# Kernel tuning notes

Measured on AMD Instinct MI355X. Metric: run time of the kernel, lower is better.

## Reference

```python
import jax, jax.numpy as jnp
import numpy as np
from jax import lax

EPS = 1e-5
K = 16  # MixedOp.self.k


def conv(x, w, stride=1, pad=0, dil=1, groups=1):
    return lax.conv_general_dilated(
        x, w, (stride, stride), [(pad, pad), (pad, pad)],
        rhs_dilation=(dil, dil), feature_group_count=groups,
        dimension_numbers=('NCHW', 'OIHW', 'NCHW'))


def bn(x):
    # BatchNorm2d(affine=False) in training mode: normalize with batch stats
    m = jnp.mean(x, axis=(0, 2, 3), keepdims=True)
    v = jnp.var(x, axis=(0, 2, 3), keepdims=True)
    return (x - m) * lax.rsqrt(v + EPS)


def maxpool3(x):
    return lax.reduce_window(x, -jnp.inf, lax.max, (1, 1, 3, 3), (1, 1, 1, 1),
                             [(0, 0), (0, 0), (1, 1), (1, 1)])


def avgpool3(x):
    # AvgPool2d(3, stride=1, padding=1, count_include_pad=False)
    s = lax.reduce_window(x, 0., lax.add, (1, 1, 3, 3), (1, 1, 1, 1),
                          [(0, 0), (0, 0), (1, 1), (1, 1)])
    c = lax.reduce_window(jnp.ones_like(x), 0., lax.add, (1, 1, 3, 3),
                          (1, 1, 1, 1), [(0, 0), (0, 0), (1, 1), (1, 1)])
    return s / c


def sep_conv(x, dw1, pw1, dw2, pw2):
    C = x.shape[1]
    p = dw1.shape[-1] // 2
    h = jax.nn.relu(x)
    h = conv(h, dw1, pad=p, groups=C)
    h = bn(conv(h, pw1))
    h = jax.nn.relu(h)
    h = conv(h, dw2, pad=p, groups=C)
    return bn(conv(h, pw2))


def dil_conv(x, dw, pw):
    C = x.shape[1]
    p = (dw.shape[-1] // 2) * 2  # dilation=2 padding (3x3->2, 5x5->4)
    h = jax.nn.relu(x)
    h = conv(h, dw, pad=p, dil=2, groups=C)
    return bn(conv(h, pw))


def setup_inputs() -> dict:
    key = jax.random.key(0)
    C, B, H, W = 256, 32, 64, 64
    c_op = C // K  # 16 channels fed to each candidate op
    ks = jax.random.split(key, 17)
    g = lambda k, shp, fan: jax.random.normal(k, shp, jnp.float32) / np.sqrt(fan)
    return {
        'x': jax.random.normal(ks[0], (B, C, H, W), jnp.float32),
        # ChannelAttention se: 1x1 convs, reduction=2
        'ca_w1': g(ks[1], (C // 2, C, 1, 1), C),
        'ca_w2': g(ks[2], (C, C // 2, 1, 1), C // 2),
        # sep_conv_3x3 (two dw+pw stages)
        's3_dw1': g(ks[3], (c_op, 1, 3, 3), 9),
        's3_pw1': g(ks[4], (c_op, c_op, 1, 1), c_op),
        's3_dw2': g(ks[5], (c_op, 1, 3, 3), 9),
        's3_pw2': g(ks[6], (c_op, c_op, 1, 1), c_op),
        # sep_conv_5x5
        's5_dw1': g(ks[7], (c_op, 1, 5, 5), 25),
        's5_pw1': g(ks[8], (c_op, c_op, 1, 1), c_op),
        's5_dw2': g(ks[9], (c_op, 1, 5, 5), 25),
        's5_pw2': g(ks[10], (c_op, c_op, 1, 1), c_op),
        # dil_conv_3x3 / dil_conv_5x5
        'd3_dw': g(ks[11], (c_op, 1, 3, 3), 9),
        'd3_pw': g(ks[12], (c_op, c_op, 1, 1), c_op),
        'd5_dw': g(ks[13], (c_op, 1, 5, 5), 25),
        'd5_pw': g(ks[14], (c_op, c_op, 1, 1), c_op),
        # AttentionModule fc: channel = 8*c_op = 128, ratio = 8
        'at_w1': g(ks[15], (c_op, 8 * c_op), 8 * c_op),  # Linear(128->16)
        'at_w2': g(ks[16], (8 * c_op, c_op), c_op),      # Linear(16->128)
    }


def reference(x, ca_w1, ca_w2, s3_dw1, s3_pw1, s3_dw2, s3_pw2,
              s5_dw1, s5_pw1, s5_dw2, s5_pw2, d3_dw, d3_pw, d5_dw, d5_pw,
              at_w1, at_w2):
    B, C, H, W = x.shape
    c_sel = C // K  # number of selected channels (16)

    # ---- ChannelAttention ----
    mx = jnp.max(x, axis=(2, 3), keepdims=True)   # [B,C,1,1]
    av = jnp.mean(x, axis=(2, 3), keepdims=True)
    se = lambda z: conv(jax.nn.relu(conv(z, ca_w1)), ca_w2)
    num_list = jax.nn.sigmoid(se(mx) + se(av))    # [B,C,1,1]

    aux = x                                       # auxiliary_op = Identity (stride=1)
    xg = x * num_list

    # ---- top-k channel routing ----
    slist = jnp.sum(num_list, axis=0).reshape(C)  # sum over batch
    _, idx = lax.top_k(slist, c_sel)              # sorted, largest first
    xt = xg[:, idx]                               # gather [B,c_sel,H,W]

    # ---- 8 candidate branches (DARTS PRIMITIVES, stride=1) ----
    branches = [
        jnp.zeros_like(xt),                       # none
        bn(maxpool3(xt)),                         # max_pool_3x3 + BN
        bn(avgpool3(xt)),                         # avg_pool_3x3 + BN
        xt,                                       # skip_connect (Identity)
        sep_conv(xt, s3_dw1, s3_pw1, s3_dw2, s3_pw2),
        sep_conv(xt, s5_dw1, s5_pw1, s5_dw2, s5_pw2),
        dil_conv(xt, d3_dw, d3_pw),
        dil_conv(xt, d5_dw, d5_pw),
    ]
    temp = jnp.concatenate(branches, axis=1)      # [B, 8*c_sel, H, W]

    # ---- AttentionModule ----
    y = jnp.mean(temp, axis=(2, 3))               # [B, 8*c_sel]
    y = jax.nn.sigmoid(jax.nn.relu(y @ at_w1.T) @ at_w2.T)
    att = temp * y[:, :, None, None]
    op_attention = jnp.sum(y.reshape(B, 8, c_sel), axis=(0, 2))  # [8]

    # sum the 8 branch chunks
    out = jnp.sum(att.reshape(B, 8, c_sel, H, W), axis=1)

    # scatter back into gated x, then residual add
    xg = xg.at[:, idx].set(out)
    return xg + aux, op_attention
```

## Files before the change

### kernel.cpp

```cpp
#include <hip/hip_runtime.h>
#include <math.h>

static constexpr int B = 32, C = 256, HW = 4096, CS = 16;
static constexpr int BHW = B * HW;
static constexpr size_t IMG = (size_t)B * CS * HW;

static constexpr size_t OFF_S     = 0;
static constexpr size_t OFF_SQ    = 4096;
static constexpr size_t OFF_U     = 8192;
static constexpr size_t ACC_FLOATS= 8256;
static constexpr size_t OFF_MX    = 8256;
static constexpr size_t OFF_AV    = OFF_MX + 8192;
static constexpr size_t OFF_NUM   = OFF_AV + 8192;
static constexpr size_t OFF_Y     = OFF_NUM + 8192;
static constexpr size_t OFF_ACO   = OFF_Y + 4096;
static constexpr size_t OFF_BIAS  = OFF_ACO + 4096;
static constexpr size_t OFF_INT   = OFF_BIAS + 512;
static constexpr size_t OFF_R     = 42112;

__device__ inline float wave_sum(float v) {
  v += __shfl_down(v, 32); v += __shfl_down(v, 16); v += __shfl_down(v, 8);
  v += __shfl_down(v, 4);  v += __shfl_down(v, 2);  v += __shfl_down(v, 1);
  return v;
}
__device__ inline float wave_max(float v) {
  v = fmaxf(v, __shfl_down(v, 32)); v = fmaxf(v, __shfl_down(v, 16));
  v = fmaxf(v, __shfl_down(v, 8));  v = fmaxf(v, __shfl_down(v, 4));
  v = fmaxf(v, __shfl_down(v, 2));  v = fmaxf(v, __shfl_down(v, 1));
  return v;
}

__global__ __launch_bounds__(256) void k_stats(const float4* __restrict__ x,
                                               float* __restrict__ mx, float* __restrict__ av) {
  int bc = blockIdx.x;
  const float4* p = x + (size_t)bc * 1024;
  float mmax = -INFINITY, msum = 0.f;
  for (int i = threadIdx.x; i < 1024; i += 256) {
    float4 v = p[i];
    mmax = fmaxf(mmax, fmaxf(fmaxf(v.x, v.y), fmaxf(v.z, v.w)));
    msum += v.x + v.y + v.z + v.w;
  }
  __shared__ float rs[4], rm[4];
  float s = wave_sum(msum), m = wave_max(mmax);
  int w = threadIdx.x >> 6;
  if ((threadIdx.x & 63) == 0) { rs[w] = s; rm[w] = m; }
  __syncthreads();
  if (threadIdx.x == 0) {
    mx[bc] = fmaxf(fmaxf(rm[0], rm[1]), fmaxf(rm[2], rm[3]));
    av[bc] = (rs[0] + rs[1] + rs[2] + rs[3]) * (1.f / 4096.f);
  }
}

__global__ __launch_bounds__(128) void k_se(const float* __restrict__ mx, const float* __restrict__ av,
                                            const float* __restrict__ w1, const float* __restrict__ w2,
                                            float* __restrict__ num) {
  int b = blockIdx.x, t = threadIdx.x;
  __shared__ float zs[2][256], h[2][128];
  for (int i = t; i < 256; i += 128) { zs[0][i] = mx[b * 256 + i]; zs[1][i] = av[b * 256 + i]; }
  __syncthreads();
  {
    const float* wr = w1 + (size_t)t * 256;
    float am = 0.f, aa = 0.f;
    for (int i = 0; i < 256; i++) { float w = wr[i]; am = fmaf(w, zs[0][i], am); aa = fmaf(w, zs[1][i], aa); }
    h[0][t] = fmaxf(am, 0.f); h[1][t] = fmaxf(aa, 0.f);
  }
  __syncthreads();
  for (int c = t; c < 256; c += 128) {
    const float* wr = w2 + (size_t)c * 128;
    float sm = 0.f, sa = 0.f;
    for (int j = 0; j < 128; j++) { float w = wr[j]; sm = fmaf(w, h[0][j], sm); sa = fmaf(w, h[1][j], sa); }
    float s = sm + sa;
    num[b * 256 + c] = 1.f / (1.f + expf(-s));
  }
}

__global__ __launch_bounds__(256) void k_select(const float* __restrict__ num,
                                                int* __restrict__ idx, int* __restrict__ selmap,
                                                float* __restrict__ accbase) {
  __shared__ float s[256];
  int t = threadIdx.x;
  for (int i = t; i < (int)ACC_FLOATS; i += 256) accbase[i] = 0.f;
  float acc = 0.f;
  for (int b = 0; b < B; b++) acc += num[b * 256 + t];
  s[t] = acc; selmap[t] = -1;
  __syncthreads();
  float v = s[t];
  int rank = 0;
  for (int c = 0; c < 256; c++) {
    float o = s[c];
    rank += (o > v) || (o == v && c < t);
  }
  if (rank < 16) { idx[rank] = t; selmap[t] = rank; }
}

template<int KK, int DIL, int BN>
__device__ __forceinline__ void dw_full(const float* __restrict__ src, float sc,
                                        const float* __restrict__ w, float* __restrict__ dst,
                                        float* lt, float mu, float rs) {
  constexpr int P = (KK / 2) * DIL, TW = 64 + 2 * P;
  float wr[KK * KK];
#pragma unroll
  for (int i = 0; i < KK * KK; i++) wr[i] = w[i];
  for (int i = threadIdx.x; i < TW * TW; i += 256) {
    int ty = i / TW, tx = i - ty * TW;
    int y = ty - P, xx = tx - P;
    float v = 0.f;
    if ((unsigned)y < 64u && (unsigned)xx < 64u) {
      v = src[y * 64 + xx] * sc;
      if (BN) v = (v - mu) * rs;
      v = fmaxf(v, 0.f);
    }
    lt[i] = v;
  }
  __syncthreads();
  for (int i = threadIdx.x; i < HW; i += 256) {
    int y = i >> 6, xx = i & 63;
    const float* t0 = lt + y * TW + xx;
    float acc = 0.f;
#pragma unroll
    for (int a = 0; a < KK; a++)
#pragma unroll
      for (int q = 0; q < KK; q++)
        acc = fmaf(wr[a * KK + q], t0[a * DIL * TW + q * DIL], acc);
    dst[i] = acc;
  }
}

__device__ __forceinline__ void pools_full(const float* __restrict__ src, float sc,
                                           float* __restrict__ dmax, float* __restrict__ davg,
                                           float* __restrict__ S, float* __restrict__ SQ,
                                           int bk, float* lt, float* red) {
  for (int i = threadIdx.x; i < HW; i += 256) lt[i] = src[i] * sc;
  __syncthreads();
  float s1 = 0.f, q1 = 0.f, s2 = 0.f, q2 = 0.f, s3 = 0.f;
  for (int i = threadIdx.x; i < HW; i += 256) {
    int y = i >> 6, xx = i & 63;
    int y0 = max(y - 1, 0), y1 = min(y + 1, 63), x0 = max(xx - 1, 0), x1 = min(xx + 1, 63);
    float mx = -INFINITY, sm = 0.f;
    for (int yy = y0; yy <= y1; yy++)
      for (int cx = x0; cx <= x1; cx++) { float v = lt[yy * 64 + cx]; mx = fmaxf(mx, v); sm += v; }
    float av = sm / (float)((y1 - y0 + 1) * (x1 - x0 + 1));
    dmax[i] = mx; davg[i] = av;
    s1 += mx; q1 += mx * mx; s2 += av; q2 += av * av; s3 += lt[i];
  }
  s1 = wave_sum(s1); q1 = wave_sum(q1); s2 = wave_sum(s2); q2 = wave_sum(q2); s3 = wave_sum(s3);
  int w = threadIdx.x >> 6;
  if ((threadIdx.x & 63) == 0) { red[w] = s1; red[4 + w] = q1; red[8 + w] = s2; red[12 + w] = q2; red[16 + w] = s3; }
  __syncthreads();
  if (threadIdx.x == 0) {
    S[512 + bk]  = red[0] + red[1] + red[2] + red[3];
    SQ[512 + bk] = red[4] + red[5] + red[6] + red[7];
    S[1024 + bk] = red[8] + red[9] + red[10] + red[11];
    SQ[1024 + bk]= red[12] + red[13] + red[14] + red[15];
    S[1536 + bk] = red[16] + red[17] + red[18] + red[19];
  }
}

__global__ __launch_bounds__(256) void k_branchA(
    const float* __restrict__ x, const float* __restrict__ num, const int* __restrict__ idx,
    const float* __restrict__ d3dw, const float* __restrict__ d5dw,
    const float* __restrict__ s3dw1, const float* __restrict__ s5dw1,
    float* __restrict__ R, float* __restrict__ scr,
    float* __restrict__ S, float* __restrict__ SQ) {
  __shared__ float lt[72 * 72];
  __shared__ float red[20];
  int blk = blockIdx.x;
  int op = blk / 512, bk = blk - op * 512;
  int b = bk >> 4, k = bk & 15;
  int c = idx[k];
  float sc = num[b * 256 + c];
  const float* src = x + ((size_t)b * 256 + c) * HW;
  size_t o = (size_t)bk * HW;
  switch (op) {
    case 0: pools_full(src, sc, R + o, R + IMG + o, S, SQ, bk, lt, red); break;
    case 1: dw_full<3, 2, 0>(src, sc, d3dw + k * 9,  scr + 0 * IMG + o, lt, 0.f, 0.f); break;
    case 2: dw_full<5, 2, 0>(src, sc, d5dw + k * 25, scr + 1 * IMG + o, lt, 0.f, 0.f); break;
    case 3: dw_full<3, 1, 0>(src, sc, s3dw1 + k * 9,  scr + 2 * IMG + o, lt, 0.f, 0.f); break;
    case 4: dw_full<5, 1, 0>(src, sc, s5dw1 + k * 25, scr + 3 * IMG + o, lt, 0.f, 0.f); break;
  }
}

__device__ __forceinline__ void pw_tile(const float* __restrict__ in, const float* __restrict__ w16,
                                        float* __restrict__ out, float* __restrict__ sacc,
                                        float* __restrict__ qacc, int perB, int b, int tile,
                                        float* wsh, float* redS, float* redQ) {
  int t = threadIdx.x;
  wsh[t] = w16[t];
  size_t base = (size_t)b * 16 * HW + tile * 256;
  float sv[16];
#pragma unroll
  for (int i = 0; i < 16; i++) sv[i] = in[base + (size_t)i * HW + t];
  __syncthreads();
  int wv = t >> 6, lane = t & 63;
#pragma unroll
  for (int cc = 0; cc < 16; cc++) {
    float acc = 0.f;
#pragma unroll
    for (int i = 0; i < 16; i++) acc = fmaf(wsh[cc * 16 + i], sv[i], acc);
    out[base + (size_t)cc * HW + t] = acc;
    float s = wave_sum(acc), q = wave_sum(acc * acc);
    if (lane == 0) { redS[cc * 4 + wv] = s; redQ[cc * 4 + wv] = q; }
  }
  __syncthreads();
  if (t < 16) {
    float s = redS[t * 4] + redS[t * 4 + 1] + redS[t * 4 + 2] + redS[t * 4 + 3];
    float q = redQ[t * 4] + redQ[t * 4 + 1] + redQ[t * 4 + 2] + redQ[t * 4 + 3];
    int sl = perB ? b * 16 + t : t;
    atomicAdd(&sacc[sl], s); atomicAdd(&qacc[sl], q);
  }
}

__global__ __launch_bounds__(256) void k_branchB(
    const float* __restrict__ scr,
    const float* __restrict__ d3pw, const float* __restrict__ d5pw,
    const float* __restrict__ s3pw1, const float* __restrict__ s5pw1,
    float* __restrict__ R, float* __restrict__ t3, float* __restrict__ t5,
    float* __restrict__ S, float* __restrict__ SQ, float* __restrict__ U) {
  __shared__ float wsh[256], redS[64], redQ[64];
  int blk = blockIdx.x;
  int op = blk >> 9, rem = blk & 511;
  int b = rem >> 4, tile = rem & 15;
  switch (op) {
    case 0: pw_tile(scr + 0 * IMG, d3pw,  R + 4 * IMG, S + 6 * 512, SQ + 6 * 512, 1, b, tile, wsh, redS, redQ); break;
    case 1: pw_tile(scr + 1 * IMG, d5pw,  R + 5 * IMG, S + 7 * 512, SQ + 7 * 512, 1, b, tile, wsh, redS, redQ); break;
    case 2: pw_tile(scr + 2 * IMG, s3pw1, t3, U + 0,  U + 16, 0, b, tile, wsh, redS, redQ); break;
    case 3: pw_tile(scr + 3 * IMG, s5pw1, t5, U + 32, U + 48, 0, b, tile, wsh, redS, redQ); break;
  }
}

__global__ __launch_bounds__(256) void k_branchC(
    const float* __restrict__ t3, const float* __restrict__ t5,
    const float* __restrict__ s3dw2, const float* __restrict__ s5dw2,
    float* __restrict__ scr, const float* __restrict__ U) {
  __shared__ float lt[68 * 68];
  int blk = blockIdx.x;
  int op = blk >> 9, bk = blk & 511, k = bk & 15;
  size_t o = (size_t)bk * HW;
  if (op == 0) {
    float mu = U[k] * (1.f / (float)BHW);
    float var = U[16 + k] * (1.f / (float)BHW) - mu * mu;
    float rs = rsqrtf(var + 1e-5f);
    dw_full<3, 1, 1>(t3 + o, 1.f, s3dw2 + k * 9, scr + 0 * IMG + o, lt, mu, rs);
  } else {
    float mu = U[32 + k] * (1.f / (float)BHW);
    float var = U[48 + k] * (1.f / (float)BHW) - mu * mu;
    float rs = rsqrtf(var + 1e-5f);
    dw_full<5, 1, 1>(t5 + o, 1.f, s5dw2 + k * 25, scr + 1 * IMG + o, lt, mu, rs);
  }
}

__global__ __launch_bounds__(256) void k_branchD(
    const float* __restrict__ scr,
    const float* __restrict__ s3pw2, const float* __restrict__ s5pw2,
    float* __restrict__ R, float* __restrict__ S, float* __restrict__ SQ) {
  __shared__ float wsh[256], redS[64], redQ[64];
  int blk = blockIdx.x;
  int op = blk >> 9, rem = blk & 511;
  int b = rem >> 4, tile = rem & 15;
  if (op == 0) pw_tile(scr + 0 * IMG, s3pw2, R + 2 * IMG, S + 4 * 512, SQ + 4 * 512, 1, b, tile, wsh, redS, redQ);
  else         pw_tile(scr + 1 * IMG, s5pw2, R + 3 * IMG, S + 5 * 512, SQ + 5 * 512, 1, b, tile, wsh, redS, redQ);
}

__global__ __launch_bounds__(128) void k_att(const float* __restrict__ S, const float* __restrict__ SQ,
                                             const float* __restrict__ w1, const float* __restrict__ w2,
                                             float* __restrict__ y, float* __restrict__ aco,
                                             float* __restrict__ bia) {
  int b = blockIdx.x, t = threadIdx.x;
  __shared__ float ym[128], h[16], msh[8][16], rssh[8][16], ysh[128];
  int op = t >> 4, k = t & 15;
  bool isbn = (op == 1 || op == 2 || op >= 4);
  float m = 0.f, rsc = 0.f;
  {
    float ss = 0.f, qq = 0.f;
    for (int bb = 0; bb < B; bb++) { ss += S[op * 512 + bb * 16 + k]; qq += SQ[op * 512 + bb * 16 + k]; }
    if (isbn) {
      m = ss * (1.f / (float)BHW);
      float var = qq * (1.f / (float)BHW) - m * m;
      rsc = rsqrtf(var + 1e-5f);
    }
  }
  msh[op][k] = m; rssh[op][k] = rsc;
  float sm = S[op * 512 + b * 16 + k] * (1.f / 4096.f);
  float yme = (op == 0) ? 0.f : ((op == 3) ? sm : (sm - m) * rsc);
  ym[t] = yme;
  __syncthreads();
  if (t < 16) {
    const float* wr = w1 + (size_t)t * 128;
    float acc = 0.f;
    for (int c = 0; c < 128; c++) acc = fmaf(wr[c], ym[c], acc);
    h[t] = fmaxf(acc, 0.f);
  }
  __syncthreads();
  {
    const float* wr = w2 + (size_t)t * 16;
    float acc = 0.f;
    for (int j = 0; j < 16; j++) acc = fmaf(wr[j], h[j], acc);
    float yy = 1.f / (1.f + expf(-acc));
    ysh[t] = yy; y[b * 128 + t] = yy;
  }
  __syncthreads();
  if (t < 16) {
    float bias = 0.f;
    for (int o2 = 1; o2 < 8; o2++) {
      float yv = ysh[o2 * 16 + t];
      float a;
      if (o2 == 3) a = yv;
      else { a = yv * rssh[o2][t]; bias -= yv * rssh[o2][t] * msh[o2][t]; }
      aco[(b * 16 + t) * 8 + o2] = a;
    }
    bia[b * 16 + t] = bias;
  }
}

__global__ __launch_bounds__(256) void k_final(const float* __restrict__ x, const float* __restrict__ num,
                                               const int* __restrict__ selmap, const int* __restrict__ idx,
                                               const float* __restrict__ rbuf, const float* __restrict__ aco,
                                               const float* __restrict__ bia, const float* __restrict__ ybuf,
                                               float* __restrict__ out, float* __restrict__ out8) {
  __shared__ float sh[256];
  int bc = blockIdx.x;
  if (bc == B * C) {
    int t = threadIdx.x, op = t >> 5, lane = t & 31;
    float acc = 0.f;
    for (int i = lane; i < 512; i += 32) { int bb = i >> 4, kk = i & 15; acc += ybuf[bb * 128 + op * 16 + kk]; }
    sh[t] = acc;
    __syncthreads();
    if (lane == 0) {
      float s = 0.f;
      for (int i = 0; i < 32; i++) s += sh[op * 32 + i];
      out8[op] = s;
    }
    return;
  }
  int b = bc >> 8;
  int k = selmap[bc & 255];
  const float4* xs = (const float4*)(x + (size_t)bc * HW);
  float4* od = (float4*)(out + (size_t)bc * HW);
  if (k < 0) {
    float sc = 1.f + num[bc];
    for (int i = threadIdx.x; i < 1024; i += 256) {
      float4 v = xs[i];
      v.x *= sc; v.y *= sc; v.z *= sc; v.w *= sc;
      od[i] = v;
    }
  } else {
    int bk = b * 16 + k;
    int ci = idx[k];
    float scn = num[b * 256 + ci];
    const float4* xtp = (const float4*)(x + ((size_t)b * 256 + ci) * HW);
    const float4* r0 = (const float4*)(rbuf + ((size_t)0 * 512 + bk) * HW);
    const float4* r1 = (const float4*)(rbuf + ((size_t)1 * 512 + bk) * HW);
    const float4* r2 = (const float4*)(rbuf + ((size_t)2 * 512 + bk) * HW);
    const float4* r3 = (const float4*)(rbuf + ((size_t)3 * 512 + bk) * HW);
    const float4* r4 = (const float4*)(rbuf + ((size_t)4 * 512 + bk) * HW);
    const float4* r5 = (const float4*)(rbuf + ((size_t)5 * 512 + bk) * HW);
    float a1 = aco[bk * 8 + 1], a2 = aco[bk * 8 + 2], a3 = aco[bk * 8 + 3] * scn, a4 = aco[bk * 8 + 4];
    float a5 = aco[bk * 8 + 5], a6 = aco[bk * 8 + 6], a7 = aco[bk * 8 + 7];
    float bias = bia[bk];
    for (int i = threadIdx.x; i < 1024; i += 256) {
      float4 xv = xs[i], tv = xtp[i];
      float4 v0 = r0[i], v1 = r1[i], v2 = r2[i], v3 = r3[i], v4 = r4[i], v5 = r5[i];
      float4 o;
      o.x = xv.x + bias + a1 * v0.x + a2 * v1.x + a3 * tv.x + a4 * v2.x + a5 * v3.x + a6 * v4.x + a7 * v5.x;
      o.y = xv.y + bias + a1 * v0.y + a2 * v1.y + a3 * tv.y + a4 * v2.y + a5 * v3.y + a6 * v4.y + a7 * v5.y;
      o.z = xv.z + bias + a1 * v0.z + a2 * v1.z + a3 * tv.z + a4 * v2.z + a5 * v3.z + a6 * v4.z + a7 * v5.z;
      o.w = xv.w + bias + a1 * v0.w + a2 * v1.w + a3 * tv.w + a4 * v2.w + a5 * v3.w + a6 * v4.w + a7 * v5.w;
      od[i] = o;
    }
  }
}

extern "C" void kernel_launch(void* const* d_in, const int* in_sizes, int n_in,
                              void* d_out, int out_size, void* d_ws, size_t ws_size,
                              hipStream_t stream) {
  const float* x      = (const float*)d_in[0];
  const float* ca_w1  = (const float*)d_in[1];
  const float* ca_w2  = (const float*)d_in[2];
  const float* s3_dw1 = (const float*)d_in[3];
  const float* s3_pw1 = (const float*)d_in[4];
  const float* s3_dw2 = (const float*)d_in[5];
  const float* s3_pw2 = (const float*)d_in[6];
  const float* s5_dw1 = (const float*)d_in[7];
  const float* s5_pw1 = (const float*)d_in[8];
  const float* s5_dw2 = (const float*)d_in[9];
  const float* s5_pw2 = (const float*)d_in[10];
  const float* d3_dw  = (const float*)d_in[11];
  const float* d3_pw  = (const float*)d_in[12];
  const float* d5_dw  = (const float*)d_in[13];
  const float* d5_pw  = (const float*)d_in[14];
  const float* at_w1  = (const float*)d_in[15];
  const float* at_w2  = (const float*)d_in[16];

  float* ws = (float*)d_ws;
  float* S = ws + OFF_S;  float* SQ = ws + OFF_SQ;  float* U = ws + OFF_U;
  float* mx = ws + OFF_MX; float* av = ws + OFF_AV; float* num = ws + OFF_NUM;
  float* ybuf = ws + OFF_Y; float* aco = ws + OFF_ACO; float* bia = ws + OFF_BIAS;
  int* ib = (int*)(ws + OFF_INT);
  int* idx = ib; int* selmap = ib + 16;
  float* R = ws + OFF_R;

  float* outf = (float*)d_out;
  float* scr = outf;
  float* t3  = outf + 4 * IMG;
  float* t5  = outf + 5 * IMG;
  float* out8 = outf + (size_t)B * C * HW;

  k_stats<<<B * C, 256, 0, stream>>>((const float4*)x, mx, av);
  k_se<<<B, 128, 0, stream>>>(mx, av, ca_w1, ca_w2, num);
  k_select<<<1, 256, 0, stream>>>(num, idx, selmap, ws);
  k_branchA<<<5 * 512, 256, 0, stream>>>(x, num, idx, d3_dw, d5_dw, s3_dw1, s5_dw1, R, scr, S, SQ);
  k_branchB<<<4 * 512, 256, 0, stream>>>(scr, d3_pw, d5_pw, s3_pw1, s5_pw1, R, t3, t5, S, SQ, U);
  k_branchC<<<2 * 512, 256, 0, stream>>>(t3, t5, s3_dw2, s5_dw2, scr, U);
  k_branchD<<<2 * 512, 256, 0, stream>>>(scr, s3_pw2, s5_pw2, R, S, SQ);
  k_att<<<B, 128, 0, stream>>>(S, SQ, at_w1, at_w2, ybuf, aco, bia);
  k_final<<<B * C + 1, 256, 0, stream>>>(x, num, selmap, idx, R, aco, bia, ybuf, outf, out8);
}
```

Baseline: 213.6 us.

## Fuse SE and top-k selection, share halo tile across branch-A ops

Merges the SE MLP and channel top-k into one kernel, using an atomic counter so the last block does the selection. The accumulator zeroing moves into block 0 of the stats kernel. Branch A now loads each selected channel's 72x72 padded tile once and runs pools plus all four depthwise convs from it, and the pointwise stages process all ops per block. This cuts launches and redundant global reads of x, but leaves far fewer blocks (512) with more serial work each, which may reduce parallelism on a large GPU.

```diff
diff --git a/kernel.cpp b/kernel.cpp
--- a/kernel.cpp
+++ b/kernel.cpp
@@ -5,18 +5,19 @@
 static constexpr int BHW = B * HW;
 static constexpr size_t IMG = (size_t)B * CS * HW;
 
-static constexpr size_t OFF_S     = 0;
-static constexpr size_t OFF_SQ    = 4096;
-static constexpr size_t OFF_U     = 8192;
-static constexpr size_t ACC_FLOATS= 8256;
-static constexpr size_t OFF_MX    = 8256;
-static constexpr size_t OFF_AV    = OFF_MX + 8192;
-static constexpr size_t OFF_NUM   = OFF_AV + 8192;
-static constexpr size_t OFF_Y     = OFF_NUM + 8192;
-static constexpr size_t OFF_ACO   = OFF_Y + 4096;
-static constexpr size_t OFF_BIAS  = OFF_ACO + 4096;
-static constexpr size_t OFF_INT   = OFF_BIAS + 512;
-static constexpr size_t OFF_R     = 42112;
+static constexpr size_t OFF_S    = 0;
+static constexpr size_t OFF_SQ   = 4096;
+static constexpr size_t OFF_U    = 8192;
+static constexpr size_t OFF_CNT  = 8256;
+static constexpr size_t ACC_END  = 8260;
+static constexpr size_t OFF_MX   = 8320;
+static constexpr size_t OFF_AV   = OFF_MX + 8192;
+static constexpr size_t OFF_NUM  = OFF_AV + 8192;
+static constexpr size_t OFF_Y    = OFF_NUM + 8192;
+static constexpr size_t OFF_ACO  = OFF_Y + 4096;
+static constexpr size_t OFF_BIAS = OFF_ACO + 4096;
+static constexpr size_t OFF_INT  = OFF_BIAS + 512;
+static constexpr size_t OFF_R    = OFF_INT + 384;
 
 __device__ inline float wave_sum(float v) {
   v += __shfl_down(v, 32); v += __shfl_down(v, 16); v += __shfl_down(v, 8);
@@ -31,8 +32,10 @@
 }
 
 __global__ __launch_bounds__(256) void k_stats(const float4* __restrict__ x,
-                                               float* __restrict__ mx, float* __restrict__ av) {
+                                               float* __restrict__ mx, float* __restrict__ av,
+                                               float* __restrict__ accbase) {
   int bc = blockIdx.x;
+  if (bc == 0) for (int i = threadIdx.x; i < (int)ACC_END; i += 256) accbase[i] = 0.f;
   const float4* p = x + (size_t)bc * 1024;
   float mmax = -INFINITY, msum = 0.f;
   for (int i = threadIdx.x; i < 1024; i += 256) {
@@ -51,112 +54,49 @@
   }
 }
 
-__global__ __launch_bounds__(128) void k_se(const float* __restrict__ mx, const float* __restrict__ av,
-                                            const float* __restrict__ w1, const float* __restrict__ w2,
-                                            float* __restrict__ num) {
+__global__ __launch_bounds__(256) void k_sesel(const float* __restrict__ mx, const float* __restrict__ av,
+                                               const float* __restrict__ w1, const float* __restrict__ w2,
+                                               float* __restrict__ num,
+                                               int* __restrict__ idx, int* __restrict__ selmap,
+                                               unsigned* __restrict__ cnt) {
+  __shared__ float zs0[256], zs1[256], h0[128], h1[128];
+  __shared__ unsigned lastv;
   int b = blockIdx.x, t = threadIdx.x;
-  __shared__ float zs[2][256], h[2][128];
-  for (int i = t; i < 256; i += 128) { zs[0][i] = mx[b * 256 + i]; zs[1][i] = av[b * 256 + i]; }
-  __syncthreads();
-  {
+  zs0[t] = mx[b * 256 + t]; zs1[t] = av[b * 256 + t];
+  __syncthreads();
+  if (t < 128) {
     const float* wr = w1 + (size_t)t * 256;
     float am = 0.f, aa = 0.f;
-    for (int i = 0; i < 256; i++) { float w = wr[i]; am = fmaf(w, zs[0][i], am); aa = fmaf(w, zs[1][i], aa); }
-    h[0][t] = fmaxf(am, 0.f); h[1][t] = fmaxf(aa, 0.f);
-  }
-  __syncthreads();
-  for (int c = t; c < 256; c += 128) {
-    const float* wr = w2 + (size_t)c * 128;
+    for (int i = 0; i < 256; i++) { float w = wr[i]; am = fmaf(w, zs0[i], am); aa = fmaf(w, zs1[i], aa); }
+    h0[t] = fmaxf(am, 0.f); h1[t] = fmaxf(aa, 0.f);
+  }
+  __syncthreads();
+  {
+    const float* wr = w2 + (size_t)t * 128;
     float sm = 0.f, sa = 0.f;
-    for (int j = 0; j < 128; j++) { float w = wr[j]; sm = fmaf(w, h[0][j], sm); sa = fmaf(w, h[1][j], sa); }
-    float s = sm + sa;
-    num[b * 256 + c] = 1.f / (1.f + expf(-s));
-  }
-}
-
-__global__ __launch_bounds__(256) void k_select(const float* __restrict__ num,
-                                                int* __restrict__ idx, int* __restrict__ selmap,
-                                                float* __restrict__ accbase) {
-  __shared__ float s[256];
-  int t = threadIdx.x;
-  for (int i = t; i < (int)ACC_FLOATS; i += 256) accbase[i] = 0.f;
-  float acc = 0.f;
-  for (int b = 0; b < B; b++) acc += num[b * 256 + t];
-  s[t] = acc; selmap[t] = -1;
-  __syncthreads();
-  float v = s[t];
-  int rank = 0;
-  for (int c = 0; c < 256; c++) {
-    float o = s[c];
-    rank += (o > v) || (o == v && c < t);
-  }
-  if (rank < 16) { idx[rank] = t; selmap[t] = rank; }
-}
-
-template<int KK, int DIL, int BN>
-__device__ __forceinline__ void dw_full(const float* __restrict__ src, float sc,
-                                        const float* __restrict__ w, float* __restrict__ dst,
-                                        float* lt, float mu, float rs) {
-  constexpr int P = (KK / 2) * DIL, TW = 64 + 2 * P;
-  float wr[KK * KK];
-#pragma unroll
-  for (int i = 0; i < KK * KK; i++) wr[i] = w[i];
-  for (int i = threadIdx.x; i < TW * TW; i += 256) {
-    int ty = i / TW, tx = i - ty * TW;
-    int y = ty - P, xx = tx - P;
-    float v = 0.f;
-    if ((unsigned)y < 64u && (unsigned)xx < 64u) {
-      v = src[y * 64 + xx] * sc;
-      if (BN) v = (v - mu) * rs;
-      v = fmaxf(v, 0.f);
-    }
-    lt[i] = v;
-  }
-  __syncthreads();
-  for (int i = threadIdx.x; i < HW; i += 256) {
-    int y = i >> 6, xx = i & 63;
-    const float* t0 = lt + y * TW + xx;
-    float acc = 0.f;
-#pragma unroll
-    for (int a = 0; a < KK; a++)
-#pragma unroll
-      for (int q = 0; q < KK; q++)
-        acc = fmaf(wr[a * KK + q], t0[a * DIL * TW + q * DIL], acc);
-    dst[i] = acc;
-  }
-}
-
-__device__ __forceinline__ void pools_full(const float* __restrict__ src, float sc,
-                                           float* __restrict__ dmax, float* __restrict__ davg,
-                                           float* __restrict__ S, float* __restrict__ SQ,
-                                           int bk, float* lt, float* red) {
-  for (int i = threadIdx.x; i < HW; i += 256) lt[i] = src[i] * sc;
-  __syncthreads();
-  float s1 = 0.f, q1 = 0.f, s2 = 0.f, q2 = 0.f, s3 = 0.f;
-  for (int i = threadIdx.x; i < HW; i += 256) {
-    int y = i >> 6, xx = i & 63;
-    int y0 = max(y - 1, 0), y1 = min(y + 1, 63), x0 = max(xx - 1, 0), x1 = min(xx + 1, 63);
-    float mx = -INFINITY, sm = 0.f;
-    for (int yy = y0; yy <= y1; yy++)
-      for (int cx = x0; cx <= x1; cx++) { float v = lt[yy * 64 + cx]; mx = fmaxf(mx, v); sm += v; }
-    float av = sm / (float)((y1 - y0 + 1) * (x1 - x0 + 1));
-    dmax[i] = mx; davg[i] = av;
-    s1 += mx; q1 += mx * mx; s2 += av; q2 += av * av; s3 += lt[i];
-  }
-  s1 = wave_sum(s1); q1 = wave_sum(q1); s2 = wave_sum(s2); q2 = wave_sum(q2); s3 = wave_sum(s3);
-  int w = threadIdx.x >> 6;
-  if ((threadIdx.x & 63) == 0) { red[w] = s1; red[4 + w] = q1; red[8 + w] = s2; red[12 + w] = q2; red[16 + w] = s3; }
-  __syncthreads();
-  if (threadIdx.x == 0) {
-    S[512 + bk]  = red[0] + red[1] + red[2] + red[3];
-    SQ[512 + bk] = red[4] + red[5] + red[6] + red[7];
-    S[1024 + bk] = red[8] + red[9] + red[10] + red[11];
-    SQ[1024 + bk]= red[12] + red[13] + red[14] + red[15];
-    S[1536 + bk] = red[16] + red[17] + red[18] + red[19];
-  }
-}
-
-__global__ __launch_bounds__(256) void k_branchA(
+    for (int j = 0; j < 128; j++) { float w = wr[j]; sm = fmaf(w, h0[j], sm); sa = fmaf(w, h1[j], sa); }
+    num[b * 256 + t] = 1.f / (1.f + expf(-(sm + sa)));
+  }
+  __threadfence();
+  if (t == 0) lastv = atomicAdd(cnt, 1u);
+  __syncthreads();
+  if (lastv == 31u) {
+    __threadfence();
+    float acc = 0.f;
+    for (int bb = 0; bb < B; bb++) acc += num[bb * 256 + t];
+    zs0[t] = acc; selmap[t] = -1;
+    __syncthreads();
+    float v = zs0[t];
+    int rank = 0;
+    for (int c = 0; c < 256; c++) {
+      float o = zs0[c];
+      rank += (o > v) || (o == v && c < t);
+    }
+    if (rank < 16) { idx[rank] = t; selmap[t] = rank; }
+  }
+}
+
+__global__ __launch_bounds__(256) void k_fuseA(
     const float* __restrict__ x, const float* __restrict__ num, const int* __restrict__ idx,
     const float* __restrict__ d3dw, const float* __restrict__ d5dw,
     const float* __restrict__ s3dw1, const float* __restrict__ s5dw1,
@@ -164,34 +104,123 @@
     float* __restrict__ S, float* __restrict__ SQ) {
   __shared__ float lt[72 * 72];
   __shared__ float red[20];
-  int blk = blockIdx.x;
-  int op = blk / 512, bk = blk - op * 512;
-  int b = bk >> 4, k = bk & 15;
-  int c = idx[k];
-  float sc = num[b * 256 + c];
+  const int t = threadIdx.x;
+  const int bk = blockIdx.x, b = bk >> 4, k = bk & 15;
+  const int c = idx[k];
+  const float sc = num[b * 256 + c];
   const float* src = x + ((size_t)b * 256 + c) * HW;
-  size_t o = (size_t)bk * HW;
-  switch (op) {
-    case 0: pools_full(src, sc, R + o, R + IMG + o, S, SQ, bk, lt, red); break;
-    case 1: dw_full<3, 2, 0>(src, sc, d3dw + k * 9,  scr + 0 * IMG + o, lt, 0.f, 0.f); break;
-    case 2: dw_full<5, 2, 0>(src, sc, d5dw + k * 25, scr + 1 * IMG + o, lt, 0.f, 0.f); break;
-    case 3: dw_full<3, 1, 0>(src, sc, s3dw1 + k * 9,  scr + 2 * IMG + o, lt, 0.f, 0.f); break;
-    case 4: dw_full<5, 1, 0>(src, sc, s5dw1 + k * 25, scr + 3 * IMG + o, lt, 0.f, 0.f); break;
-  }
-}
-
-__device__ __forceinline__ void pw_tile(const float* __restrict__ in, const float* __restrict__ w16,
-                                        float* __restrict__ out, float* __restrict__ sacc,
-                                        float* __restrict__ qacc, int perB, int b, int tile,
-                                        float* wsh, float* redS, float* redQ) {
+  const size_t o = (size_t)bk * HW;
+  for (int i = t; i < 72 * 72; i += 256) {
+    int ty = i / 72, tx = i - ty * 72;
+    int y = ty - 4, xx = tx - 4;
+    float v = 0.f;
+    if ((unsigned)y < 64u && (unsigned)xx < 64u) v = src[y * 64 + xx] * sc;
+    lt[i] = v;
+  }
+  __syncthreads();
+  {
+    float s1 = 0.f, q1 = 0.f, s2 = 0.f, q2 = 0.f, s3 = 0.f;
+    for (int i = t; i < HW; i += 256) {
+      int y = i >> 6, xx = i & 63;
+      const float* ctr = lt + (y + 4) * 72 + (xx + 4);
+      int dy0 = (y > 0) ? -1 : 0, dy1 = (y < 63) ? 1 : 0;
+      int dx0 = (xx > 0) ? -1 : 0, dx1 = (xx < 63) ? 1 : 0;
+      float mxv = -INFINITY, sm = 0.f;
+      for (int dy = dy0; dy <= dy1; dy++)
+        for (int dx = dx0; dx <= dx1; dx++) { float v = ctr[dy * 72 + dx]; mxv = fmaxf(mxv, v); sm += v; }
+      float avv = sm / (float)((dy1 - dy0 + 1) * (dx1 - dx0 + 1));
+      R[o + i] = mxv; R[IMG + o + i] = avv;
+      s1 += mxv; q1 += mxv * mxv; s2 += avv; q2 += avv * avv; s3 += ctr[0];
+    }
+    s1 = wave_sum(s1); q1 = wave_sum(q1); s2 = wave_sum(s2); q2 = wave_sum(q2); s3 = wave_sum(s3);
+    int w = t >> 6;
+    if ((t & 63) == 0) { red[w] = s1; red[4 + w] = q1; red[8 + w] = s2; red[12 + w] = q2; red[16 + w] = s3; }
+    __syncthreads();
+    if (t == 0) {
+      S[512 + bk]  = red[0] + red[1] + red[2] + red[3];
+      SQ[512 + bk] = red[4] + red[5] + red[6] + red[7];
+      S[1024 + bk] = red[8] + red[9] + red[10] + red[11];
+      SQ[1024 + bk]= red[12] + red[13] + red[14] + red[15];
+      S[1536 + bk] = red[16] + red[17] + red[18] + red[19];
+    }
+  }
+  {
+    float w[9];
+#pragma unroll
+    for (int i = 0; i < 9; i++) w[i] = d3dw[k * 9 + i];
+    for (int i = t; i < HW; i += 256) {
+      int y = i >> 6, xx = i & 63;
+      const float* ctr = lt + (y + 4) * 72 + (xx + 4);
+      float acc = 0.f;
+#pragma unroll
+      for (int a = 0; a < 3; a++)
+#pragma unroll
+        for (int q = 0; q < 3; q++)
+          acc = fmaf(w[a * 3 + q], fmaxf(ctr[(2 * a - 2) * 72 + (2 * q - 2)], 0.f), acc);
+      scr[0 * IMG + o + i] = acc;
+    }
+  }
+  {
+    float w[25];
+#pragma unroll
+    for (int i = 0; i < 25; i++) w[i] = d5dw[k * 25 + i];
+    for (int i = t; i < HW; i += 256) {
+      int y = i >> 6, xx = i & 63;
+      const float* ctr = lt + (y + 4) * 72 + (xx + 4);
+      float acc = 0.f;
+#pragma unroll
+      for (int a = 0; a < 5; a++)
+#pragma unroll
+        for (int q = 0; q < 5; q++)
+          acc = fmaf(w[a * 5 + q], fmaxf(ctr[(2 * a - 4) * 72 + (2 * q - 4)], 0.f), acc);
+      scr[1 * IMG + o + i] = acc;
+    }
+  }
+  {
+    float w[9];
+#pragma unroll
+    for (int i = 0; i < 9; i++) w[i] = s3dw1[k * 9 + i];
+    for (int i = t; i < HW; i += 256) {
+      int y = i >> 6, xx = i & 63;
+      const float* ctr = lt + (y + 4) * 72 + (xx + 4);
+      float acc = 0.f;
+#pragma unroll
+      for (int a = 0; a < 3; a++)
+#pragma unroll
+        for (int q = 0; q < 3; q++)
+          acc = fmaf(w[a * 3 + q], fmaxf(ctr[(a - 1) * 72 + (q - 1)], 0.f), acc);
+      scr[2 * IMG + o + i] = acc;
+    }
+  }
+  {
+    float w[25];
+#pragma unroll
+    for (int i = 0; i < 25; i++) w[i] = s5dw1[k * 25 + i];
+    for (int i = t; i < HW; i += 256) {
+      int y = i >> 6, xx = i & 63;
+      const float* ctr = lt + (y + 4) * 72 + (xx + 4);
+      float acc = 0.f;
+#pragma unroll
+      for (int a = 0; a < 5; a++)
+#pragma unroll
+        for (int q = 0; q < 5; q++)
+          acc = fmaf(w[a * 5 + q], fmaxf(ctr[(a - 2) * 72 + (q - 2)], 0.f), acc);
+      scr[3 * IMG + o + i] = acc;
+    }
+  }
+}
+
+__device__ __forceinline__ void do_pw(const float* __restrict__ in, const float* __restrict__ wsh,
+                                      float* __restrict__ out, float* __restrict__ sacc,
+                                      float* __restrict__ qacc, int perB, int b, int tile,
+                                      float* redS, float* redQ) {
   int t = threadIdx.x;
-  wsh[t] = w16[t];
   size_t base = (size_t)b * 16 * HW + tile * 256;
   float sv[16];
 #pragma unroll
   for (int i = 0; i < 16; i++) sv[i] = in[base + (size_t)i * HW + t];
-  __syncthreads();
   int wv = t >> 6, lane = t & 63;
+  __syncthreads();
 #pragma unroll
   for (int cc = 0; cc < 16; cc++) {
     float acc = 0.f;
@@ -210,25 +239,55 @@
   }
 }
 
-__global__ __launch_bounds__(256) void k_branchB(
+__global__ __launch_bounds__(256) void k_fuseB(
     const float* __restrict__ scr,
     const float* __restrict__ d3pw, const float* __restrict__ d5pw,
     const float* __restrict__ s3pw1, const float* __restrict__ s5pw1,
     float* __restrict__ R, float* __restrict__ t3, float* __restrict__ t5,
     float* __restrict__ S, float* __restrict__ SQ, float* __restrict__ U) {
-  __shared__ float wsh[256], redS[64], redQ[64];
-  int blk = blockIdx.x;
-  int op = blk >> 9, rem = blk & 511;
-  int b = rem >> 4, tile = rem & 15;
-  switch (op) {
-    case 0: pw_tile(scr + 0 * IMG, d3pw,  R + 4 * IMG, S + 6 * 512, SQ + 6 * 512, 1, b, tile, wsh, redS, redQ); break;
-    case 1: pw_tile(scr + 1 * IMG, d5pw,  R + 5 * IMG, S + 7 * 512, SQ + 7 * 512, 1, b, tile, wsh, redS, redQ); break;
-    case 2: pw_tile(scr + 2 * IMG, s3pw1, t3, U + 0,  U + 16, 0, b, tile, wsh, redS, redQ); break;
-    case 3: pw_tile(scr + 3 * IMG, s5pw1, t5, U + 32, U + 48, 0, b, tile, wsh, redS, redQ); break;
-  }
-}
-
-__global__ __launch_bounds__(256) void k_branchC(
+  __shared__ float wall[1024], redS[64], redQ[64];
+  int t = threadIdx.x;
+  int b = blockIdx.x >> 4, tile = blockIdx.x & 15;
+  wall[t] = d3pw[t]; wall[256 + t] = d5pw[t]; wall[512 + t] = s3pw1[t]; wall[768 + t] = s5pw1[t];
+  do_pw(scr + 0 * IMG, wall + 0,   R + 4 * IMG, S + 6 * 512, SQ + 6 * 512, 1, b, tile, redS, redQ);
+  do_pw(scr + 1 * IMG, wall + 256, R + 5 * IMG, S + 7 * 512, SQ + 7 * 512, 1, b, tile, redS, redQ);
+  do_pw(scr + 2 * IMG, wall + 512, t3, U + 0,  U + 16, 0, b, tile, redS, redQ);
+  do_pw(scr + 3 * IMG, wall + 768, t5, U + 32, U + 48, 0, b, tile, redS, redQ);
+}
+
+template<int KK, int BN>
+__device__ __forceinline__ void dw_one(const float* __restrict__ src, const float* __restrict__ w,
+                                       float* __restrict__ dst, float* lt, float mu, float rs) {
+  constexpr int P = KK / 2, TW = 64 + 2 * P;
+  float wr[KK * KK];
+#pragma unroll
+  for (int i = 0; i < KK * KK; i++) wr[i] = w[i];
+  for (int i = threadIdx.x; i < TW * TW; i += 256) {
+    int ty = i / TW, tx = i - ty * TW;
+    int y = ty - P, xx = tx - P;
+    float v = 0.f;
+    if ((unsigned)y < 64u && (unsigned)xx < 64u) {
+      v = src[y * 64 + xx];
+      if (BN) v = (v - mu) * rs;
+      v = fmaxf(v, 0.f);
+    }
+    lt[i] = v;
+  }
+  __syncthreads();
+  for (int i = threadIdx.x; i < HW; i += 256) {
+    int y = i >> 6, xx = i & 63;
+    const float* t0 = lt + y * TW + xx;
+    float acc = 0.f;
+#pragma unroll
+    for (int a = 0; a < KK; a++)
+#pragma unroll
+      for (int q = 0; q < KK; q++)
+        acc = fmaf(wr[a * KK + q], t0[a * TW + q], acc);
+    dst[i] = acc;
+  }
+}
+
+__global__ __launch_bounds__(256) void k_fuseC(
     const float* __restrict__ t3, const float* __restrict__ t5,
     const float* __restrict__ s3dw2, const float* __restrict__ s5dw2,
     float* __restrict__ scr, const float* __restrict__ U) {
@@ -239,26 +298,24 @@
   if (op == 0) {
     float mu = U[k] * (1.f / (float)BHW);
     float var = U[16 + k] * (1.f / (float)BHW) - mu * mu;
-    float rs = rsqrtf(var + 1e-5f);
-    dw_full<3, 1, 1>(t3 + o, 1.f, s3dw2 + k * 9, scr + 0 * IMG + o, lt, mu, rs);
+    dw_one<3, 1>(t3 + o, s3dw2 + k * 9, scr + 0 * IMG + o, lt, mu, rsqrtf(var + 1e-5f));
   } else {
     float mu = U[32 + k] * (1.f / (float)BHW);
     float var = U[48 + k] * (1.f / (float)BHW) - mu * mu;
-    float rs = rsqrtf(var + 1e-5f);
-    dw_full<5, 1, 1>(t5 + o, 1.f, s5dw2 + k * 25, scr + 1 * IMG + o, lt, mu, rs);
-  }
-}
-
-__global__ __launch_bounds__(256) void k_branchD(
+    dw_one<5, 1>(t5 + o, s5dw2 + k * 25, scr + 1 * IMG + o, lt, mu, rsqrtf(var + 1e-5f));
+  }
+}
+
+__global__ __launch_bounds__(256) void k_fuseD(
     const float* __restrict__ scr,
     const float* __restrict__ s3pw2, const float* __restrict__ s5pw2,
     float* __restrict__ R, float* __restrict__ S, float* __restrict__ SQ) {
-  __shared__ float wsh[256], redS[64], redQ[64];
-  int blk = blockIdx.x;
-  int op = blk >> 9, rem = blk & 511;
-  int b = rem >> 4, tile = rem & 15;
-  if (op == 0) pw_tile(scr + 0 * IMG, s3pw2, R + 2 * IMG, S + 4 * 512, SQ + 4 * 512, 1, b, tile, wsh, redS, redQ);
-  else         pw_tile(scr + 1 * IMG, s5pw2, R + 3 * IMG, S + 5 * 512, SQ + 5 * 512, 1, b, tile, wsh, redS, redQ);
+  __shared__ float wall[512], redS[64], redQ[64];
+  int t = threadIdx.x;
+  int b = blockIdx.x >> 4, tile = blockIdx.x & 15;
+  wall[t] = s3pw2[t]; wall[256 + t] = s5pw2[t];
+  do_pw(scr + 0 * IMG, wall + 0,   R + 2 * IMG, S + 4 * 512, SQ + 4 * 512, 1, b, tile, redS, redQ);
+  do_pw(scr + 1 * IMG, wall + 256, R + 3 * IMG, S + 5 * 512, SQ + 5 * 512, 1, b, tile, redS, redQ);
 }
 
 __global__ __launch_bounds__(128) void k_att(const float* __restrict__ S, const float* __restrict__ SQ,
@@ -393,6 +450,7 @@
 
   float* ws = (float*)d_ws;
   float* S = ws + OFF_S;  float* SQ = ws + OFF_SQ;  float* U = ws + OFF_U;
+  unsigned* cnt = (unsigned*)(ws + OFF_CNT);
   float* mx = ws + OFF_MX; float* av = ws + OFF_AV; float* num = ws + OFF_NUM;
   float* ybuf = ws + OFF_Y; float* aco = ws + OFF_ACO; float* bia = ws + OFF_BIAS;
   int* ib = (int*)(ws + OFF_INT);
@@ -405,13 +463,12 @@
   float* t5  = outf + 5 * IMG;
   float* out8 = outf + (size_t)B * C * HW;
 
-  k_stats<<<B * C, 256, 0, stream>>>((const float4*)x, mx, av);
-  k_se<<<B, 128, 0, stream>>>(mx, av, ca_w1, ca_w2, num);
-  k_select<<<1, 256, 0, stream>>>(num, idx, selmap, ws);
-  k_branchA<<<5 * 512, 256, 0, stream>>>(x, num, idx, d3_dw, d5_dw, s3_dw1, s5_dw1, R, scr, S, SQ);
-  k_branchB<<<4 * 512, 256, 0, stream>>>(scr, d3_pw, d5_pw, s3_pw1, s5_pw1, R, t3, t5, S, SQ, U);
-  k_branchC<<<2 * 512, 256, 0, stream>>>(t3, t5, s3_dw2, s5_dw2, scr, U);
-  k_branchD<<<2 * 512, 256, 0, stream>>>(scr, s3_pw2, s5_pw2, R, S, SQ);
+  k_stats<<<B * C, 256, 0, stream>>>((const float4*)x, mx, av, ws);
+  k_sesel<<<B, 256, 0, stream>>>(mx, av, ca_w1, ca_w2, num, idx, selmap, cnt);
+  k_fuseA<<<512, 256, 0, stream>>>(x, num, idx, d3_dw, d5_dw, s3_dw1, s5_dw1, R, scr, S, SQ);
+  k_fuseB<<<512, 256, 0, stream>>>(scr, d3_pw, d5_pw, s3_pw1, s5_pw1, R, t3, t5, S, SQ, U);
+  k_fuseC<<<2 * 512, 256, 0, stream>>>(t3, t5, s3_dw2, s5_dw2, scr, U);
+  k_fuseD<<<512, 256, 0, stream>>>(scr, s3_pw2, s5_pw2, R, S, SQ);
   k_att<<<B, 128, 0, stream>>>(S, SQ, at_w1, at_w2, ybuf, aco, bia);
   k_final<<<B * C + 1, 256, 0, stream>>>(x, num, selmap, idx, R, aco, bia, ybuf, outf, out8);
 }
```

New measurement: 218.4 us. 2.3% more time.
